# Optimization experiments

Measured on AMD Instinct MI355X. Metric: run time of the kernel, lower is better.

Reference implementation:

```python
import jax, jax.numpy as jnp
import numpy as np

E = 1024

def setup_inputs() -> dict:
    key = jax.random.key(0)
    ks = jax.random.split(key, 9)
    s = 1.0 / np.sqrt(E)
    return {
        "x": jax.random.normal(ks[0], (4, 2048, E), dtype=jnp.float32),
        "Wq": jax.random.uniform(ks[1], (E, E), jnp.float32, -s, s),
        "bq": jax.random.uniform(ks[2], (E,), jnp.float32, -s, s),
        "Wk": jax.random.uniform(ks[3], (E, E), jnp.float32, -s, s),
        "bk": jax.random.uniform(ks[4], (E,), jnp.float32, -s, s),
        "Wv": jax.random.uniform(ks[5], (E, E), jnp.float32, -s, s),
        "bv": jax.random.uniform(ks[6], (E,), jnp.float32, -s, s),
        "Wo": jax.random.uniform(ks[7], (E, E), jnp.float32, -s, s),
        "bo": jax.random.uniform(ks[8], (E,), jnp.float32, -s, s),
    }

def reference(x, Wq, bq, Wk, bk, Wv, bv, Wo, bo):
    # Note: the torch module never splits heads; attention is over full embed_dim.
    # nn.Linear: y = x @ W.T + b
    Q = jnp.einsum('bse,fe->bsf', x, Wq) + bq
    K = jnp.einsum('bse,fe->bsf', x, Wk) + bk
    V = jnp.einsum('bse,fe->bsf', x, Wv) + bv
    scale = 1.0 / jnp.sqrt(jnp.asarray(x.shape[-1], x.dtype))
    scores = jnp.einsum('bqe,bke->bqk', Q, K) * scale  # [B, S, S]
    weights = jax.nn.softmax(scores, axis=-1)
    out = jnp.einsum('bqk,bke->bqe', weights, V)
    # dropout is identity in eval mode
    return jnp.einsum('bse,fe->bsf', out, Wo) + bo
```

## Files before the change

### kernel.cpp

```cpp
#include <hip/hip_runtime.h>
#include <hip/hip_bf16.h>
#include <stdint.h>

typedef short bf16x8 __attribute__((ext_vector_type(8)));
typedef float f32x4 __attribute__((ext_vector_type(4)));
typedef __attribute__((address_space(3))) void lds_void_t;
typedef __attribute__((address_space(1))) void g_void_t;

static __device__ __forceinline__ unsigned short f2b(float f) {
    __hip_bfloat16 b = __float2bfloat16(f);
    return __builtin_bit_cast(unsigned short, b);
}
static __device__ __forceinline__ float b2f(unsigned int u) {
    return __builtin_bit_cast(float, u << 16);
}

__global__ __launch_bounds__(256) void prep(
    const float* __restrict__ x,
    const float* __restrict__ wq, const float* __restrict__ wk,
    const float* __restrict__ wv, const float* __restrict__ wo,
    const float* __restrict__ bq, const float* __restrict__ bk,
    const float* __restrict__ bv_, float* __restrict__ bqkv,
    ushort* __restrict__ xb, ushort* __restrict__ wqkvb)
{
    const int T = 3145728;
    int i = blockIdx.x * 256 + threadIdx.x;
    const int stride = gridDim.x * 256;
    for (; i < T; i += stride) {
        const float* src; ushort* dst; int off;
        if (i < 2097152) { src = x; dst = xb; off = i; }
        else {
            const int j = i - 2097152;
            const int w = j >> 18;
            off = j & 262143;
            src = (w == 0) ? wq : (w == 1) ? wk : (w == 2) ? wv : wo;
            dst = wqkvb + (w << 20);
        }
        float4 v = reinterpret_cast<const float4*>(src)[off];
        ushort4 o;
        o.x = f2b(v.x); o.y = f2b(v.y); o.z = f2b(v.z); o.w = f2b(v.w);
        reinterpret_cast<ushort4*>(dst)[off] = o;
    }
    const int t = blockIdx.x * 256 + threadIdx.x;
    if (t < 3072) {
        const int sec = t >> 10, of = t & 1023;
        bqkv[t] = sec == 0 ? bq[of] : (sec == 1 ? bk[of] : bv_[of]);
    }
}

template<bool HAS_BIAS>
__global__ __launch_bounds__(512, 2)
void gemm256_bt(const ushort* __restrict__ A, const ushort* __restrict__ B,
                const float* __restrict__ bias, ushort* __restrict__ C,
                int lda, int ldb, int ldc, int K,
                long strideA, long strideB, long strideC, float alpha)
{
    __shared__ __align__(16) ushort smem[2][2][16384];

    const int bz = blockIdx.z;
    A += (size_t)bz * strideA;
    B += (size_t)bz * strideB;
    C += (size_t)bz * strideC;

    const int gx = gridDim.x, gy = gridDim.y;
    const int nwg = gx * gy;
    int bx = blockIdx.x, by = blockIdx.y;
    if ((nwg & 7) == 0) {
        const int flat = blockIdx.x + gx * blockIdx.y;
        const int cpx = nwg >> 3;
        const int u = (flat & 7) * cpx + (flat >> 3);
        bx = u % gx;
        by = u / gx;
    }

    const int tid = threadIdx.x;
    const int w   = tid >> 6;
    const int l   = tid & 63;
    const int wr  = w >> 2;
    const int wc  = w & 3;

    const int bRow = by * 256;
    const int bCol = bx * 256;

    const int lr   = l >> 3;
    const int scol = (((l & 7) ^ lr) << 3);

    f32x4 acc[8][4];
#pragma unroll
    for (int m = 0; m < 8; ++m)
#pragma unroll
        for (int n = 0; n < 4; ++n)
            acc[m][n] = f32x4{0.f, 0.f, 0.f, 0.f};

    const int NT = K >> 6;

#pragma unroll
    for (int p = 0; p < 4; ++p) {
        const int c = w * 4 + p;
        const ushort* gA = A + (size_t)(bRow + c * 8 + lr) * lda + scol;
        const ushort* gB = B + (size_t)(bCol + c * 8 + lr) * ldb + scol;
        __builtin_amdgcn_global_load_lds((const g_void_t*)gA,
            (lds_void_t*)((char*)&smem[0][0][0] + c * 1024), 16, 0, 0);
        __builtin_amdgcn_global_load_lds((const g_void_t*)gB,
            (lds_void_t*)((char*)&smem[0][1][0] + c * 1024), 16, 0, 0);
    }
    __syncthreads();

    int cur = 0;
    bf16x8 af[4][2], bfr[2][2];
    for (int t = 0; t < NT; ++t) {
        const char* sAc = (const char*)&smem[cur][0][0];
        const char* sBc = (const char*)&smem[cur][1][0];
        char* sAn = (char*)&smem[cur ^ 1][0][0];
        char* sBn = (char*)&smem[cur ^ 1][1][0];
        const int k1  = (t + 1) << 6;
        const bool pre = (t + 1 < NT);

#pragma unroll
        for (int p = 0; p < 4; ++p) {
            const int mh = p >> 1;
            const int nh = (p == 1 || p == 2) ? 1 : 0;
            if (p == 0 || p == 2) {
#pragma unroll
                for (int i = 0; i < 4; ++i) {
                    const int ar = wr * 128 + (mh * 4 + i) * 16 + (l & 15);
#pragma unroll
                    for (int ks = 0; ks < 2; ++ks) {
                        const int slot = (ks * 4 + (l >> 4)) ^ (ar & 7);
                        af[i][ks] = *reinterpret_cast<const bf16x8*>(
                            sAc + ar * 128 + slot * 16);
                    }
                }
            }
            if (p != 2) {
#pragma unroll
                for (int j = 0; j < 2; ++j) {
                    const int br = wc * 64 + (nh * 2 + j) * 16 + (l & 15);
#pragma unroll
                    for (int ks = 0; ks < 2; ++ks) {
                        const int slot = (ks * 4 + (l >> 4)) ^ (br & 7);
                        bfr[j][ks] = *reinterpret_cast<const bf16x8*>(
                            sBc + br * 128 + slot * 16);
                    }
                }
            }
            if (pre) {
                const int c = w * 4 + p;
                const ushort* gA = A + (size_t)(bRow + c * 8 + lr) * lda + (k1 + scol);
                const ushort* gB = B + (size_t)(bCol + c * 8 + lr) * ldb + (k1 + scol);
                __builtin_amdgcn_global_load_lds((const g_void_t*)gA,
                    (lds_void_t*)(sAn + c * 1024), 16, 0, 0);
                __builtin_amdgcn_global_load_lds((const g_void_t*)gB,
                    (lds_void_t*)(sBn + c * 1024), 16, 0, 0);
            }
            __builtin_amdgcn_s_setprio(1);
#pragma unroll
            for (int ks = 0; ks < 2; ++ks)
#pragma unroll
                for (int i = 0; i < 4; ++i)
#pragma unroll
                    for (int j = 0; j < 2; ++j)
                        acc[mh * 4 + i][nh * 2 + j] =
                            __builtin_amdgcn_mfma_f32_16x16x32_bf16(
                                af[i][ks], bfr[j][ks],
                                acc[mh * 4 + i][nh * 2 + j], 0, 0, 0);
            __builtin_amdgcn_s_setprio(0);
            __builtin_amdgcn_sched_barrier(0);
        }
        __syncthreads();
        cur ^= 1;
    }

    ushort* st = (ushort*)smem;
    const int cl = l & 15;
#pragma unroll
    for (int n = 0; n < 4; ++n) {
        const int col = wc * 64 + n * 16 + cl;
        const float bv = HAS_BIAS ? bias[bCol + col] : 0.f;
#pragma unroll
        for (int m = 0; m < 8; ++m) {
            const int row0 = wr * 128 + m * 16 + (l >> 4) * 4;
#pragma unroll
            for (int r = 0; r < 4; ++r) {
                const int row = row0 + r;
                const int sl  = ((col >> 3) ^ (row & 7));
                st[row * 256 + (sl << 3) + (col & 7)] =
                    f2b((acc[m][n][r] + bv) * alpha);
            }
        }
    }
    __syncthreads();
#pragma unroll
    for (int i = 0; i < 16; ++i) {
        const int c    = tid + (i << 9);
        const int row  = c >> 5;
        const int slot = (c & 31) ^ (row & 7);
        const uint4 v = *reinterpret_cast<const uint4*>(
            (const char*)st + row * 512 + slot * 16);
        *reinterpret_cast<uint4*>(
            C + (size_t)(bRow + row) * ldc + bCol + ((c & 31) << 3)) = v;
    }
}

template<typename CT, bool HAS_BIAS>
__global__ __launch_bounds__(256, 4)
void gemm_bt(const ushort* __restrict__ A, const ushort* __restrict__ B,
             const float* __restrict__ bias, CT* __restrict__ C,
             int lda, int ldb, int ldc, int K,
             long strideA, long strideB, long strideC, float alpha)
{
    __shared__ __align__(16) ushort smem[128 * 64 * 2];
    ushort* sA = smem;
    ushort* sB = smem + 128 * 64;

    const int bz = blockIdx.z;
    A += (size_t)bz * strideA;
    B += (size_t)bz * strideB;
    C += (size_t)bz * strideC;

    const int gx = gridDim.x, gy = gridDim.y;
    const int nwg = gx * gy;
    int bx = blockIdx.x, by = blockIdx.y;
    if ((nwg & 7) == 0) {
        const int flat = blockIdx.x + gx * blockIdx.y;
        const int cpx = nwg >> 3;
        const int u = (flat & 7) * cpx + (flat >> 3);
        bx = u % gx;
        by = u / gx;
    }

    const int tid = threadIdx.x;
    const int w   = tid >> 6;
    const int l   = tid & 63;
    const int wr  = w >> 1;
    const int wc  = w & 1;

    const int bRow = by * 128;
    const int bCol = bx * 128;

    const int lr   = l >> 3;
    const int scol = (((l & 7) ^ lr) << 3);

    f32x4 acc[4][4];
#pragma unroll
    for (int m = 0; m < 4; ++m)
#pragma unroll
        for (int n = 0; n < 4; ++n)
            acc[m][n] = f32x4{0.f, 0.f, 0.f, 0.f};

    for (int k0 = 0; k0 < K; k0 += 64) {
#pragma unroll
        for (int p = 0; p < 4; ++p) {
            const int c   = p * 4 + w;
            const int row = c * 8 + lr;
            const ushort* gA = A + (size_t)(bRow + row) * lda + (k0 + scol);
            const ushort* gB = B + (size_t)(bCol + row) * ldb + (k0 + scol);
            __builtin_amdgcn_global_load_lds((const g_void_t*)gA,
                (lds_void_t*)((char*)sA + c * 1024), 16, 0, 0);
            __builtin_amdgcn_global_load_lds((const g_void_t*)gB,
                (lds_void_t*)((char*)sB + c * 1024), 16, 0, 0);
        }
        __syncthreads();

        bf16x8 af[4][2], bfv[4][2];
#pragma unroll
        for (int m = 0; m < 4; ++m) {
            const int ar = wr * 64 + m * 16 + (l & 15);
#pragma unroll
            for (int ks = 0; ks < 2; ++ks) {
                const int slot = (ks * 4 + (l >> 4)) ^ (ar & 7);
                af[m][ks] = *reinterpret_cast<const bf16x8*>(
                    (const char*)sA + ar * 128 + slot * 16);
            }
        }
#pragma unroll
        for (int n = 0; n < 4; ++n) {
            const int br = wc * 64 + n * 16 + (l & 15);
#pragma unroll
            for (int ks = 0; ks < 2; ++ks) {
                const int slot = (ks * 4 + (l >> 4)) ^ (br & 7);
                bfv[n][ks] = *reinterpret_cast<const bf16x8*>(
                    (const char*)sB + br * 128 + slot * 16);
            }
        }
#pragma unroll
        for (int ks = 0; ks < 2; ++ks)
#pragma unroll
            for (int m = 0; m < 4; ++m)
#pragma unroll
                for (int n = 0; n < 4; ++n)
                    acc[m][n] = __builtin_amdgcn_mfma_f32_16x16x32_bf16(
                        af[m][ks], bfv[n][ks], acc[m][n], 0, 0, 0);
        __syncthreads();
    }

    const int cl = l & 15;
    if constexpr (sizeof(CT) == 2) {
        ushort* st = smem;
#pragma unroll
        for (int n = 0; n < 4; ++n) {
            const int col = wc * 64 + n * 16 + cl;
            const float bv = HAS_BIAS ? bias[bCol + col] : 0.f;
#pragma unroll
            for (int m = 0; m < 4; ++m) {
                const int row0 = wr * 64 + m * 16 + (l >> 4) * 4;
#pragma unroll
                for (int r = 0; r < 4; ++r)
                    st[(row0 + r) * 128 + col] = f2b((acc[m][n][r] + bv) * alpha);
            }
        }
        __syncthreads();
#pragma unroll
        for (int i = 0; i < 8; ++i) {
            const int c    = tid + i * 256;
            const int row  = c >> 4;
            const int col8 = (c & 15) * 8;
            *reinterpret_cast<uint4*>(
                (ushort*)C + (size_t)(bRow + row) * ldc + bCol + col8) =
                *reinterpret_cast<const uint4*>(st + row * 128 + col8);
        }
    } else {
#pragma unroll
        for (int n = 0; n < 4; ++n) {
            const int col = bCol + wc * 64 + n * 16 + cl;
            const float bv = HAS_BIAS ? bias[col] : 0.f;
#pragma unroll
            for (int m = 0; m < 4; ++m) {
#pragma unroll
                for (int r = 0; r < 4; ++r) {
                    const int row = bRow + wr * 64 + m * 16 + (l >> 4) * 4 + r;
                    ((float*)C)[(size_t)row * ldc + col] = (acc[m][n][r] + bv) * alpha;
                }
            }
        }
    }
}

__global__ __launch_bounds__(256) void softmax_rows(ushort* __restrict__ S)
{
    __shared__ float red[8];
    const size_t row = blockIdx.x;
    ushort* p = S + row * 2048;
    const int tid = threadIdx.x;

    uint4 v = reinterpret_cast<uint4*>(p)[tid];
    float f[8];
    const unsigned int* wv = reinterpret_cast<const unsigned int*>(&v);
#pragma unroll
    for (int j = 0; j < 4; ++j) {
        f[2 * j]     = b2f(wv[j] & 0xFFFFu);
        f[2 * j + 1] = b2f(wv[j] >> 16);
    }
    float mx = f[0];
#pragma unroll
    for (int j = 1; j < 8; ++j) mx = fmaxf(mx, f[j]);
#pragma unroll
    for (int s = 1; s < 64; s <<= 1) mx = fmaxf(mx, __shfl_xor(mx, s));
    if ((tid & 63) == 0) red[tid >> 6] = mx;
    __syncthreads();
    mx = fmaxf(fmaxf(red[0], red[1]), fmaxf(red[2], red[3]));

    float sum = 0.f;
#pragma unroll
    for (int j = 0; j < 8; ++j) { f[j] = __expf(f[j] - mx); sum += f[j]; }
#pragma unroll
    for (int s = 1; s < 64; s <<= 1) sum += __shfl_xor(sum, s);
    if ((tid & 63) == 0) red[4 + (tid >> 6)] = sum;
    __syncthreads();
    sum = (red[4] + red[5]) + (red[6] + red[7]);
    const float inv = 1.0f / sum;

    uint4 o;
    unsigned int* wo = reinterpret_cast<unsigned int*>(&o);
#pragma unroll
    for (int j = 0; j < 4; ++j) {
        const unsigned int lo = f2b(f[2 * j] * inv);
        const unsigned int hi = f2b(f[2 * j + 1] * inv);
        wo[j] = lo | (hi << 16);
    }
    reinterpret_cast<uint4*>(p)[tid] = o;
}

__global__ __launch_bounds__(256) void transpose_v(
    const ushort* __restrict__ V, ushort* __restrict__ Vt, int ldv, long strideV)
{
    __shared__ ushort t[64][65];
    const int b  = blockIdx.z;
    const int e0 = blockIdx.x * 64;
    const int s0 = blockIdx.y * 64;
    const int tid = threadIdx.x;
    const int cg = (tid & 15) * 4;
    const int r0 = tid >> 4;

    const ushort* Vb = V + (size_t)b * strideV;
#pragma unroll
    for (int p = 0; p < 4; ++p) {
        const int r = r0 + p * 16;
        ushort4 x = *reinterpret_cast<const ushort4*>(
            Vb + (size_t)(s0 + r) * ldv + e0 + cg);
        t[r][cg + 0] = x.x; t[r][cg + 1] = x.y;
        t[r][cg + 2] = x.z; t[r][cg + 3] = x.w;
    }
    __syncthreads();
    ushort* Vtb = Vt + (size_t)b * 1024 * 2048;
#pragma unroll
    for (int p = 0; p < 4; ++p) {
        const int e = r0 + p * 16;
        ushort4 o;
        o.x = t[cg + 0][e]; o.y = t[cg + 1][e];
        o.z = t[cg + 2][e]; o.w = t[cg + 3][e];
        *reinterpret_cast<ushort4*>(Vtb + (size_t)(e0 + e) * 2048 + s0 + cg) = o;
    }
}

extern "C" void kernel_launch(void* const* d_in, const int* in_sizes, int n_in,
                              void* d_out, int out_size, void* d_ws, size_t ws_size,
                              hipStream_t stream)
{
    const float* x  = (const float*)d_in[0];
    const float* Wq = (const float*)d_in[1];
    const float* bq = (const float*)d_in[2];
    const float* Wk = (const float*)d_in[3];
    const float* bk = (const float*)d_in[4];
    const float* Wv = (const float*)d_in[5];
    const float* bv = (const float*)d_in[6];
    const float* Wo = (const float*)d_in[7];
    const float* bo = (const float*)d_in[8];

    char* ws = (char*)d_ws;
    ushort* xb    = (ushort*)(ws);
    ushort* Wqkvb = (ushort*)(ws + 16777216);
    ushort* Wob   = Wqkvb + 3 * 1048576;
    float*  bqkv  = (float*) (ws + 25165824);
    ushort* QKVb  = (ushort*)(ws + 26214400);
    ushort* Vtb   = (ushort*)(ws + 76546048);
    ushort* Sb    = (ushort*)(ws + 93323264);
    ushort* Ob    = (ushort*)(ws + 126877696);

    prep<<<2048, 256, 0, stream>>>(x, Wq, Wk, Wv, Wo, bq, bk, bv, bqkv, xb, Wqkvb);

    gemm256_bt<true><<<dim3(12, 32, 1), 512, 0, stream>>>(
        xb, Wqkvb, bqkv, QKVb, 1024, 1024, 3072, 1024, 0, 0, 0, 1.0f);

    transpose_v<<<dim3(16, 32, 4), 256, 0, stream>>>(
        QKVb + 2048, Vtb, 3072, 2048L * 3072);

    gemm256_bt<false><<<dim3(8, 8, 4), 512, 0, stream>>>(
        QKVb, QKVb + 1024, nullptr, Sb, 3072, 3072, 2048, 1024,
        2048L * 3072, 2048L * 3072, 2048L * 2048, 0.03125f);

    softmax_rows<<<8192, 256, 0, stream>>>(Sb);

    gemm_bt<ushort, false><<<dim3(8, 16, 4), 256, 0, stream>>>(
        Sb, Vtb, nullptr, Ob, 2048, 2048, 1024, 2048,
        2048L * 2048, 1024L * 2048, 2048L * 1024, 1.0f);

    gemm_bt<float, true><<<dim3(8, 64, 1), 256, 0, stream>>>(
        Ob, Wob, bo, (float*)d_out, 1024, 1024, 1024, 1024, 0, 0, 0, 1.0f);
}
```

Before: 294.5 us.

## Fuse V transpose into QKV GEMM epilogue and restructure prefetch synchronization

```diff
diff --git a/kernel.cpp b/kernel.cpp
--- a/kernel.cpp
+++ b/kernel.cpp
@@ -49,9 +49,10 @@
 }
 
 template<bool HAS_BIAS>
-__global__ __launch_bounds__(512, 2)
+__global__ __launch_bounds__(512, 1)
 void gemm256_bt(const ushort* __restrict__ A, const ushort* __restrict__ B,
                 const float* __restrict__ bias, ushort* __restrict__ C,
+                ushort* __restrict__ Vt, int vtCol,
                 int lda, int ldb, int ldc, int K,
                 long strideA, long strideB, long strideC, float alpha)
 {
@@ -104,7 +105,6 @@
         __builtin_amdgcn_global_load_lds((const g_void_t*)gB,
             (lds_void_t*)((char*)&smem[0][1][0] + c * 1024), 16, 0, 0);
     }
-    __syncthreads();
 
     int cur = 0;
     bf16x8 af[4][2], bfr[2][2];
@@ -113,38 +113,11 @@
         const char* sBc = (const char*)&smem[cur][1][0];
         char* sAn = (char*)&smem[cur ^ 1][0][0];
         char* sBn = (char*)&smem[cur ^ 1][1][0];
-        const int k1  = (t + 1) << 6;
-        const bool pre = (t + 1 < NT);
-
-#pragma unroll
-        for (int p = 0; p < 4; ++p) {
-            const int mh = p >> 1;
-            const int nh = (p == 1 || p == 2) ? 1 : 0;
-            if (p == 0 || p == 2) {
-#pragma unroll
-                for (int i = 0; i < 4; ++i) {
-                    const int ar = wr * 128 + (mh * 4 + i) * 16 + (l & 15);
-#pragma unroll
-                    for (int ks = 0; ks < 2; ++ks) {
-                        const int slot = (ks * 4 + (l >> 4)) ^ (ar & 7);
-                        af[i][ks] = *reinterpret_cast<const bf16x8*>(
-                            sAc + ar * 128 + slot * 16);
-                    }
-                }
-            }
-            if (p != 2) {
-#pragma unroll
-                for (int j = 0; j < 2; ++j) {
-                    const int br = wc * 64 + (nh * 2 + j) * 16 + (l & 15);
-#pragma unroll
-                    for (int ks = 0; ks < 2; ++ks) {
-                        const int slot = (ks * 4 + (l >> 4)) ^ (br & 7);
-                        bfr[j][ks] = *reinterpret_cast<const bf16x8*>(
-                            sBc + br * 128 + slot * 16);
-                    }
-                }
-            }
-            if (pre) {
+
+        if (t + 1 < NT) {
+            const int k1 = (t + 1) << 6;
+#pragma unroll
+            for (int p = 0; p < 4; ++p) {
                 const int c = w * 4 + p;
                 const ushort* gA = A + (size_t)(bRow + c * 8 + lr) * lda + (k1 + scol);
                 const ushort* gB = B + (size_t)(bCol + c * 8 + lr) * ldb + (k1 + scol);
@@ -153,6 +126,42 @@
                 __builtin_amdgcn_global_load_lds((const g_void_t*)gB,
                     (lds_void_t*)(sBn + c * 1024), 16, 0, 0);
             }
+            asm volatile("s_waitcnt vmcnt(8)" ::: "memory");
+        } else {
+            asm volatile("s_waitcnt vmcnt(0)" ::: "memory");
+        }
+        __builtin_amdgcn_s_barrier();
+        __builtin_amdgcn_sched_barrier(0);
+        asm volatile("" ::: "memory");
+
+#pragma unroll
+        for (int p = 0; p < 4; ++p) {
+            const int mh = p >> 1;
+            const int nh = (p == 1 || p == 2) ? 1 : 0;
+            if (p == 0 || p == 2) {
+#pragma unroll
+                for (int i = 0; i < 4; ++i) {
+                    const int ar = wr * 128 + (mh * 4 + i) * 16 + (l & 15);
+#pragma unroll
+                    for (int ks = 0; ks < 2; ++ks) {
+                        const int slot = (ks * 4 + (l >> 4)) ^ (ar & 7);
+                        af[i][ks] = *reinterpret_cast<const bf16x8*>(
+                            sAc + ar * 128 + slot * 16);
+                    }
+                }
+            }
+            if (p != 2) {
+#pragma unroll
+                for (int j = 0; j < 2; ++j) {
+                    const int br = wc * 64 + (nh * 2 + j) * 16 + (l & 15);
+#pragma unroll
+                    for (int ks = 0; ks < 2; ++ks) {
+                        const int slot = (ks * 4 + (l >> 4)) ^ (br & 7);
+                        bfr[j][ks] = *reinterpret_cast<const bf16x8*>(
+                            sBc + br * 128 + slot * 16);
+                    }
+                }
+            }
             __builtin_amdgcn_s_setprio(1);
 #pragma unroll
             for (int ks = 0; ks < 2; ++ks)
@@ -165,40 +174,76 @@
                                 af[i][ks], bfr[j][ks],
                                 acc[mh * 4 + i][nh * 2 + j], 0, 0, 0);
             __builtin_amdgcn_s_setprio(0);
-            __builtin_amdgcn_sched_barrier(0);
+        }
+
+        asm volatile("" ::: "memory");
+        __builtin_amdgcn_sched_barrier(0);
+        __builtin_amdgcn_s_barrier();
+        cur ^= 1;
+    }
+
+    const int cl = l & 15;
+    char* stb = (char*)smem;
+    if (bCol >= vtCol) {
+#pragma unroll
+        for (int n = 0; n < 4; ++n) {
+            const int col = wc * 64 + n * 16 + cl;
+            const float bv = HAS_BIAS ? bias[bCol + col] : 0.f;
+#pragma unroll
+            for (int m = 0; m < 8; ++m) {
+                const int row0 = wr * 128 + m * 16 + (l >> 4) * 4;
+#pragma unroll
+                for (int r = 0; r < 4; ++r) {
+                    const int row = row0 + r;
+                    *(ushort*)(stb + col * 512 + ((row * 2) ^ ((col & 7) << 4))) =
+                        f2b((acc[m][n][r] + bv) * alpha);
+                }
+            }
         }
         __syncthreads();
-        cur ^= 1;
-    }
-
-    ushort* st = (ushort*)smem;
-    const int cl = l & 15;
-#pragma unroll
-    for (int n = 0; n < 4; ++n) {
-        const int col = wc * 64 + n * 16 + cl;
-        const float bv = HAS_BIAS ? bias[bCol + col] : 0.f;
-#pragma unroll
-        for (int m = 0; m < 8; ++m) {
-            const int row0 = wr * 128 + m * 16 + (l >> 4) * 4;
-#pragma unroll
-            for (int r = 0; r < 4; ++r) {
-                const int row = row0 + r;
-                const int sl  = ((col >> 3) ^ (row & 7));
-                st[row * 256 + (sl << 3) + (col & 7)] =
-                    f2b((acc[m][n][r] + bv) * alpha);
-            }
-        }
-    }
-    __syncthreads();
-#pragma unroll
-    for (int i = 0; i < 16; ++i) {
-        const int c    = tid + (i << 9);
-        const int row  = c >> 5;
-        const int slot = (c & 31) ^ (row & 7);
-        const uint4 v = *reinterpret_cast<const uint4*>(
-            (const char*)st + row * 512 + slot * 16);
-        *reinterpret_cast<uint4*>(
-            C + (size_t)(bRow + row) * ldc + bCol + ((c & 31) << 3)) = v;
+        const int bb    = bRow >> 11;
+        const int sBase = bRow & 2047;
+        const int e0    = bCol - vtCol;
+        ushort* Vtb = Vt + ((size_t)bb << 21);
+#pragma unroll
+        for (int i = 0; i < 16; ++i) {
+            const int q  = tid + (i << 9);
+            const int c  = q >> 5;
+            const int rq = (q & 31) << 4;
+            const uint4 v = *reinterpret_cast<const uint4*>(
+                stb + c * 512 + (rq ^ ((c & 7) << 4)));
+            *reinterpret_cast<uint4*>(
+                Vtb + (size_t)(e0 + c) * 2048 + sBase + ((q & 31) << 3)) = v;
+        }
+    } else {
+        ushort* st = (ushort*)smem;
+#pragma unroll
+        for (int n = 0; n < 4; ++n) {
+            const int col = wc * 64 + n * 16 + cl;
+            const float bv = HAS_BIAS ? bias[bCol + col] : 0.f;
+#pragma unroll
+            for (int m = 0; m < 8; ++m) {
+                const int row0 = wr * 128 + m * 16 + (l >> 4) * 4;
+#pragma unroll
+                for (int r = 0; r < 4; ++r) {
+                    const int row = row0 + r;
+                    const int sl  = ((col >> 3) ^ (row & 7));
+                    st[row * 256 + (sl << 3) + (col & 7)] =
+                        f2b((acc[m][n][r] + bv) * alpha);
+                }
+            }
+        }
+        __syncthreads();
+#pragma unroll
+        for (int i = 0; i < 16; ++i) {
+            const int c    = tid + (i << 9);
+            const int row  = c >> 5;
+            const int slot = (c & 31) ^ (row & 7);
+            const uint4 v = *reinterpret_cast<const uint4*>(
+                (const char*)st + row * 512 + slot * 16);
+            *reinterpret_cast<uint4*>(
+                C + (size_t)(bRow + row) * ldc + bCol + ((c & 31) << 3)) = v;
+        }
     }
 }
 
@@ -379,38 +424,6 @@
         wo[j] = lo | (hi << 16);
     }
     reinterpret_cast<uint4*>(p)[tid] = o;
-}
-
-__global__ __launch_bounds__(256) void transpose_v(
-    const ushort* __restrict__ V, ushort* __restrict__ Vt, int ldv, long strideV)
-{
-    __shared__ ushort t[64][65];
-    const int b  = blockIdx.z;
-    const int e0 = blockIdx.x * 64;
-    const int s0 = blockIdx.y * 64;
-    const int tid = threadIdx.x;
-    const int cg = (tid & 15) * 4;
-    const int r0 = tid >> 4;
-
-    const ushort* Vb = V + (size_t)b * strideV;
-#pragma unroll
-    for (int p = 0; p < 4; ++p) {
-        const int r = r0 + p * 16;
-        ushort4 x = *reinterpret_cast<const ushort4*>(
-            Vb + (size_t)(s0 + r) * ldv + e0 + cg);
-        t[r][cg + 0] = x.x; t[r][cg + 1] = x.y;
-        t[r][cg + 2] = x.z; t[r][cg + 3] = x.w;
-    }
-    __syncthreads();
-    ushort* Vtb = Vt + (size_t)b * 1024 * 2048;
-#pragma unroll
-    for (int p = 0; p < 4; ++p) {
-        const int e = r0 + p * 16;
-        ushort4 o;
-        o.x = t[cg + 0][e]; o.y = t[cg + 1][e];
-        o.z = t[cg + 2][e]; o.w = t[cg + 3][e];
-        *reinterpret_cast<ushort4*>(Vtb + (size_t)(e0 + e) * 2048 + s0 + cg) = o;
-    }
 }
 
 extern "C" void kernel_launch(void* const* d_in, const int* in_sizes, int n_in,
@@ -440,13 +453,12 @@
     prep<<<2048, 256, 0, stream>>>(x, Wq, Wk, Wv, Wo, bq, bk, bv, bqkv, xb, Wqkvb);
 
     gemm256_bt<true><<<dim3(12, 32, 1), 512, 0, stream>>>(
-        xb, Wqkvb, bqkv, QKVb, 1024, 1024, 3072, 1024, 0, 0, 0, 1.0f);
-
-    transpose_v<<<dim3(16, 32, 4), 256, 0, stream>>>(
-        QKVb + 2048, Vtb, 3072, 2048L * 3072);
+        xb, Wqkvb, bqkv, QKVb, Vtb, 2048,
+        1024, 1024, 3072, 1024, 0, 0, 0, 1.0f);
 
     gemm256_bt<false><<<dim3(8, 8, 4), 512, 0, stream>>>(
-        QKVb, QKVb + 1024, nullptr, Sb, 3072, 3072, 2048, 1024,
+        QKVb, QKVb + 1024, nullptr, Sb, nullptr, 1 << 30,
+        3072, 3072, 2048, 1024,
         2048L * 3072, 2048L * 3072, 2048L * 2048, 0.03125f);
 
     softmax_rows<<<8192, 256, 0, stream>>>(Sb);
```

Result: no change. 289.2 us (-1.8%).
